# Kernel tuning notes

Hardware: AMD Instinct MI355X
Metric: run time of the kernel (lower is better)

Reference implementation:

```python
import jax, jax.numpy as jnp
import numpy as np

N_MET = 100_000
N_RXN = 50_000
E_SUB = 2_000_000
E_ALL = 4_000_000
MSG_DIM = 16
HIDDEN = 32


def setup_inputs() -> dict:
    key = jax.random.key(0)
    ks = jax.random.split(key, 16)
    x_met = jax.random.normal(ks[0], (N_MET,), dtype=jnp.float32)
    sto_sub = jax.random.uniform(ks[1], (E_SUB,), dtype=jnp.float32, minval=0.0, maxval=1.0)
    sto_all = jax.random.normal(ks[2], (E_ALL,), dtype=jnp.float32)
    met_sub = jax.random.randint(ks[3], (E_SUB,), 0, N_MET)
    rxn_sub = jax.random.randint(ks[4], (E_SUB,), 0, N_RXN)
    met_all = jax.random.randint(ks[5], (E_ALL,), 0, N_MET)
    rxn_all = jax.random.randint(ks[6], (E_ALL,), 0, N_RXN)
    # msg_mlp: Linear(2->HIDDEN), Tanh, Linear(HIDDEN->MSG_DIM)
    W1m = jax.random.normal(ks[7], (2, HIDDEN), jnp.float32) / np.sqrt(2.0)
    b1m = jnp.zeros((HIDDEN,), jnp.float32)
    W2m = jax.random.normal(ks[8], (HIDDEN, MSG_DIM), jnp.float32) / np.sqrt(HIDDEN)
    b2m = jnp.zeros((MSG_DIM,), jnp.float32)
    # rate_mlp: Linear(MSG_DIM->HIDDEN), Tanh, Linear(HIDDEN->1)
    W1r = jax.random.normal(ks[9], (MSG_DIM, HIDDEN), jnp.float32) / np.sqrt(MSG_DIM)
    b1r = jnp.zeros((HIDDEN,), jnp.float32)
    W2r = jax.random.normal(ks[10], (HIDDEN, 1), jnp.float32) / np.sqrt(HIDDEN)
    b2r = jnp.zeros((1,), jnp.float32)
    return {
        "x_met": x_met, "sto_sub": sto_sub, "sto_all": sto_all,
        "W1m": W1m, "b1m": b1m, "W2m": W2m, "b2m": b2m,
        "W1r": W1r, "b1r": b1r, "W2r": W2r, "b2r": b2r,
        "met_sub": met_sub, "rxn_sub": rxn_sub,
        "met_all": met_all, "rxn_all": rxn_all,
    }


def reference(x_met, sto_sub, sto_all, W1m, b1m, W2m, b2m, W1r, b1r, W2r, b2r,
              met_sub, rxn_sub, met_all, rxn_all):
    # gather substrate node features and build per-edge MLP input [E_sub, 2]
    msg_in = jnp.stack([x_met[met_sub], sto_sub], axis=-1)
    # msg MLP: tanh hidden, linear out -> [E_sub, MSG_DIM]
    msg = jnp.tanh(msg_in @ W1m + b1m) @ W2m + b2m
    # scatter-add messages into reactions -> [N_RXN, MSG_DIM]
    h_rxn = jax.ops.segment_sum(msg, rxn_sub, num_segments=N_RXN)
    # rate MLP + softplus -> per-reaction rate v [N_RXN]
    v = jax.nn.softplus((jnp.tanh(h_rxn @ W1r + b1r) @ W2r + b2r)[:, 0])
    # stoichiometric contributions scattered into metabolites -> dxdt [N_MET]
    contrib = sto_all * v[rxn_all]
    dxdt = jax.ops.segment_sum(contrib, met_all, num_segments=N_MET)
    return dxdt, v
```

## Files before the change

kernel.cpp:

```cpp
#include <hip/hip_runtime.h>

#define N_MET 100000
#define N_RXN 50000
#define E_SUB 2000000
#define E_ALL 4000000
#define MSG_DIM 16
#define HIDDEN 32

#define NBKT_A 391
#define NB_ALL 489
#define NBKT_S 782
#define NB_SUB 245


__device__ __forceinline__ float fast_tanh(float x) {
    const float ax = fabsf(x);
    const float e = __expf(2.0f * ax);
    const float t = 1.0f - 2.0f * __builtin_amdgcn_rcpf(e + 1.0f);
    return copysignf(t, x);
}


__global__ __launch_bounds__(1024) void hist_pair_kernel(
    const int* __restrict__ rxn_sub, const int* __restrict__ met_all,
    int* __restrict__ histS, int* __restrict__ histA)
{
    __shared__ int hb[NBKT_S];
    const int t = threadIdx.x, bk = blockIdx.x;
    if (bk < NB_SUB) {
        for (int i = t; i < NBKT_S; i += 1024) hb[i] = 0;
        __syncthreads();
#pragma unroll
        for (int k = 0; k < 2; ++k) {
            const int i = bk * 2048 + (k << 10) + t;
            if (i < E_SUB / 4) {
                const int4 r = ((const int4*)rxn_sub)[i];
                atomicAdd(&hb[r.x >> 6], 1);
                atomicAdd(&hb[r.y >> 6], 1);
                atomicAdd(&hb[r.z >> 6], 1);
                atomicAdd(&hb[r.w >> 6], 1);
            }
        }
        __syncthreads();
        for (int i = t; i < NBKT_S; i += 1024) histS[bk * NBKT_S + i] = hb[i];
    } else {
        const int ba = bk - NB_SUB;
        for (int i = t; i < NBKT_A; i += 1024) hb[i] = 0;
        __syncthreads();
#pragma unroll
        for (int k = 0; k < 2; ++k) {
            const int i = ba * 2048 + (k << 10) + t;
            if (i < E_ALL / 4) {
                const int4 m = ((const int4*)met_all)[i];
                atomicAdd(&hb[m.x >> 8], 1);
                atomicAdd(&hb[m.y >> 8], 1);
                atomicAdd(&hb[m.z >> 8], 1);
                atomicAdd(&hb[m.w >> 8], 1);
            }
        }
        __syncthreads();
        for (int i = t; i < NBKT_A; i += 1024) histA[ba * NBKT_A + i] = hb[i];
    }
}


__global__ __launch_bounds__(256) void scan_cols_pair_kernel(
    int* __restrict__ histS, int* __restrict__ histA,
    int* __restrict__ tot_s, int* __restrict__ tot_a)
{
    __shared__ int wsum[4];
    int* hist; int* tot; int nblocks, nbkt, b;
    if ((int)blockIdx.x < NBKT_S) {
        hist = histS; tot = tot_s; nblocks = NB_SUB; nbkt = NBKT_S;
        b = blockIdx.x;
    } else {
        hist = histA; tot = tot_a; nblocks = NB_ALL; nbkt = NBKT_A;
        b = blockIdx.x - NBKT_S;
    }
    const int t = threadIdx.x, lane = t & 63, w = t >> 6;
    int carry = 0;
    for (int basei = 0; basei < nblocks; basei += 256) {
        const int bk = basei + t;
        const int val = (bk < nblocks) ? hist[(size_t)bk * nbkt + b] : 0;
        int x = val;
#pragma unroll
        for (int off = 1; off < 64; off <<= 1) {
            const int y = __shfl_up(x, off);
            if (lane >= off) x += y;
        }
        if (lane == 63) wsum[w] = x;
        __syncthreads();
        if (w == 0) {
            int s = (lane < 4) ? wsum[lane] : 0;
#pragma unroll
            for (int off = 1; off < 4; off <<= 1) {
                const int y = __shfl_up(s, off);
                if (lane >= off) s += y;
            }
            if (lane < 4) wsum[lane] = s;
        }
        __syncthreads();
        const int excl = carry + ((w > 0) ? wsum[w - 1] : 0) + x - val;
        if (bk < nblocks) hist[(size_t)bk * nbkt + b] = excl;
        carry += wsum[3];
        __syncthreads();
    }
    if (t == 0) tot[b] = carry;
}

__global__ __launch_bounds__(256) void scan_base_pair_kernel(
    const int* __restrict__ tot_s, int* __restrict__ base_s,
    const int* __restrict__ tot_a, int* __restrict__ base_a)
{
    __shared__ int wsum[4];
    const int* tot; int* base; int nbkt;
    if (blockIdx.x == 0) { tot = tot_s; base = base_s; nbkt = NBKT_S; }
    else                 { tot = tot_a; base = base_a; nbkt = NBKT_A; }
    const int t = threadIdx.x, lane = t & 63, w = t >> 6;
    int carry = 0;
    for (int basei = 0; basei < nbkt; basei += 256) {
        const int i = basei + t;
        const int val = (i < nbkt) ? tot[i] : 0;
        int x = val;
#pragma unroll
        for (int off = 1; off < 64; off <<= 1) {
            const int y = __shfl_up(x, off);
            if (lane >= off) x += y;
        }
        if (lane == 63) wsum[w] = x;
        __syncthreads();
        if (w == 0) {
            int s = (lane < 4) ? wsum[lane] : 0;
#pragma unroll
            for (int off = 1; off < 4; off <<= 1) {
                const int y = __shfl_up(s, off);
                if (lane >= off) s += y;
            }
            if (lane < 4) wsum[lane] = s;
        }
        __syncthreads();
        const int excl = carry + ((w > 0) ? wsum[w - 1] : 0) + x - val;
        if (i < nbkt) base[i] = excl;
        carry += wsum[3];
        __syncthreads();
    }
}


__global__ __launch_bounds__(1024) void scatter_bin_sub_kernel(
    const float* __restrict__ x_met, const float* __restrict__ sto_sub,
    const int* __restrict__ met_sub, const int* __restrict__ rxn_sub,
    const int* __restrict__ hist, const int* __restrict__ base,
    float2* __restrict__ pxs)
{
    __shared__ float2 se[8192];
    __shared__ int cnt[NBKT_S];
    __shared__ int loff[NBKT_S + 1];
    __shared__ int goff[NBKT_S];
    const int t = threadIdx.x, bk = blockIdx.x;
    for (int i = t; i < NBKT_S; i += 1024) {
        cnt[i] = 0;
        goff[i] = hist[bk * NBKT_S + i] + base[i];
    }
    __syncthreads();

    float2 pay[8]; int meta[8];
    const int e0 = bk * 8192;
#pragma unroll
    for (int k = 0; k < 8; ++k) {
        const int e = e0 + (k << 10) + t;
        if (e < E_SUB) {
            const int r = rxn_sub[e];
            const float x = x_met[met_sub[e]];
            const int sb = (__float_as_int(sto_sub[e]) & ~63) | (r & 63);
            pay[k] = make_float2(x, __int_as_float(sb));
            const int q = r >> 6;
            meta[k] = (atomicAdd(&cnt[q], 1) << 10) | q;
        } else meta[k] = -1;
    }
    __syncthreads();

    if (t < 64) {
        int carry = 0;
        for (int bb = 0; bb < NBKT_S; bb += 64) {
            const int idx = bb + t;
            const int val = (idx < NBKT_S) ? cnt[idx] : 0;
            int x = val;
#pragma unroll
            for (int off = 1; off < 64; off <<= 1) {
                const int y = __shfl_up(x, off);
                if (t >= off) x += y;
            }
            if (idx < NBKT_S) loff[idx] = carry + x - val;
            carry += __shfl(x, 63);
        }
        if (t == 0) loff[NBKT_S] = carry;
    }
    __syncthreads();

#pragma unroll
    for (int k = 0; k < 8; ++k) {
        if (meta[k] >= 0)
            se[loff[meta[k] & 1023] + (meta[k] >> 10)] = pay[k];
    }
    __syncthreads();

    const int w = t >> 6, lane = t & 63;
    for (int q = w; q < NBKT_S; q += 16) {
        const int s = loff[q], lenq = loff[q + 1] - s, d = goff[q];
        for (int i = lane; i < lenq; i += 64)
            pxs[d + i] = se[s + i];
    }
}

__global__ __launch_bounds__(512, 6) void bucket_msg_kernel(
    const float2* __restrict__ pxs,
    const int* __restrict__ base, const int* __restrict__ tot,
    const float* __restrict__ W1m, const float* __restrict__ b1m,
    const float* __restrict__ W2m, const float* __restrict__ b2m,
    const float* __restrict__ W1r, const float* __restrict__ b1r,
    const float* __restrict__ W2r, const float* __restrict__ b2r,
    float* __restrict__ v)
{
    __shared__ float2 se[4096];
    __shared__ float  sth[64 * 33];
    __shared__ int    cnt[64];
    __shared__ int    soff[65];
    __shared__ int    ccnt[64];
    __shared__ float  sW2m[HIDDEN * MSG_DIM];
    __shared__ float  sb2m[MSG_DIM];
    __shared__ float  sW1r[MSG_DIM * HIDDEN];
    __shared__ float  sb1r[HIDDEN];
    __shared__ float  sW2r[HIDDEN];
    __shared__ float  sb2r;
    __shared__ float  sh[64 * 17];

    const int t = threadIdx.x;
    const int w = t >> 6, l = t & 63;
    const int half = l >> 5, j = l & 31;

    for (int i = t; i < HIDDEN * MSG_DIM; i += 512) sW2m[i] = W2m[i];
    for (int i = t; i < MSG_DIM * HIDDEN; i += 512) sW1r[i] = W1r[i];
    if (t < MSG_DIM) sb2m[t] = b2m[t];
    if (t < HIDDEN) sb1r[t] = b1r[t];
    if (t >= 64 && t < 64 + HIDDEN) sW2r[t - 64] = W2r[t - 64];
    if (t == 128) sb2r = b2r[0];
    if (t < 64) ccnt[t] = 0;

    const float w1x = W1m[j];
    const float w1y = W1m[HIDDEN + j];
    const float w1b = b1m[j];

    const int b = blockIdx.x;
    const int beg = base[b];
    const int end = beg + tot[b];

    float acc[4] = {0.0f, 0.0f, 0.0f, 0.0f};

    for (int cb = beg; cb < end; cb += 4096) {
        if (t < 64) cnt[t] = 0;
        __syncthreads();

        float2 pay[8];
        int meta[8];
#pragma unroll
        for (int k = 0; k < 8; ++k) {
            const int idx = cb + t + (k << 9);
            if (idx < end) {
                const float2 pv = pxs[idx];
                const int r = __float_as_int(pv.y) & 63;
                meta[k] = (atomicAdd(&cnt[r], 1) << 6) | r;
                pay[k] = pv;
            } else meta[k] = -1;
        }
        __syncthreads();

        if (t < 64) {
            const int orig = cnt[t];
            int x = orig;
#pragma unroll
            for (int off = 1; off < 64; off <<= 1) {
                const int y = __shfl_up(x, off);
                if (t >= off) x += y;
            }
            soff[t] = x - orig;
            if (t == 63) soff[64] = x;
            ccnt[t] += orig;
        }
        __syncthreads();

#pragma unroll
        for (int k = 0; k < 8; ++k) {
            if (meta[k] >= 0)
                se[soff[meta[k] & 63] + (meta[k] >> 6)] = pay[k];
        }
        __syncthreads();

#pragma unroll
        for (int p = 0; p < 4; ++p) {
            const int q = (w << 3) + (p << 1) + half;
            const int rb = soff[q];
            const int rl = soff[q + 1] - rb;
            float a0 = 0.0f, a1 = 0.0f;
            int i = 0;
            for (; i + 2 <= rl; i += 2) {
                const float2 e0 = se[rb + i];
                const float2 e1 = se[rb + i + 1];
                a0 += fast_tanh(fmaf(e0.x, w1x, fmaf(e0.y, w1y, w1b)));
                a1 += fast_tanh(fmaf(e1.x, w1x, fmaf(e1.y, w1y, w1b)));
            }
            if (i < rl) {
                const float2 e0 = se[rb + i];
                a0 += fast_tanh(fmaf(e0.x, w1x, fmaf(e0.y, w1y, w1b)));
            }
            acc[p] += a0 + a1;
        }
        __syncthreads();
    }

#pragma unroll
    for (int p = 0; p < 4; ++p) {
        const int q = (w << 3) + (p << 1) + half;
        sth[q * 33 + j] = acc[p];
    }
    __syncthreads();

    {
        const int r = t & 63, g = (t >> 6) << 1;
        const float cntf = (float)ccnt[r];
        float h0 = cntf * sb2m[g + 0], h1 = cntf * sb2m[g + 1];
#pragma unroll 8
        for (int jj = 0; jj < HIDDEN; ++jj) {
            const float ts = sth[r * 33 + jj];
            h0 = fmaf(ts, sW2m[jj * MSG_DIM + g + 0], h0);
            h1 = fmaf(ts, sW2m[jj * MSG_DIM + g + 1], h1);
        }
        sh[r * 17 + g + 0] = h0;
        sh[r * 17 + g + 1] = h1;
    }
    __syncthreads();

    if (t < 64) {
        const int r = b * 64 + t;
        if (r < N_RXN) {
            float h[MSG_DIM];
#pragma unroll
            for (int d = 0; d < MSG_DIM; ++d) h[d] = sh[t * 17 + d];
            float acc2 = sb2r;
#pragma unroll 2
            for (int jj = 0; jj < HIDDEN; ++jj) {
                float z = sb1r[jj];
#pragma unroll
                for (int d = 0; d < MSG_DIM; ++d)
                    z = fmaf(h[d], sW1r[d * HIDDEN + jj], z);
                acc2 = fmaf(fast_tanh(z), sW2r[jj], acc2);
            }
            v[r] = fmaxf(acc2, 0.0f) + log1pf(expf(-fabsf(acc2)));
        }
    }
}


__global__ __launch_bounds__(1024) void scatter_bin_kernel(
    const float* __restrict__ sto_all, const float* __restrict__ v,
    const int* __restrict__ met_all, const int* __restrict__ rxn_all,
    const int* __restrict__ hist, const int* __restrict__ base,
    float* __restrict__ pc)
{
    __shared__ float sp[8192];
    __shared__ int cnt[NBKT_A];
    __shared__ int loff[NBKT_A + 1];
    __shared__ int goff[NBKT_A];
    const int t = threadIdx.x, bk = blockIdx.x;
    for (int i = t; i < NBKT_A; i += 1024) {
        cnt[i] = 0;
        goff[i] = hist[bk * NBKT_A + i] + base[i];
    }
    __syncthreads();

    float pay[8]; int meta[8];
    const int e0 = bk * 8192;
#pragma unroll
    for (int k = 0; k < 8; ++k) {
        const int e = e0 + (k << 10) + t;
        if (e < E_ALL) {
            const int m = met_all[e];
            const float c = sto_all[e] * v[rxn_all[e]];
            const int cb = (__float_as_int(c) & ~255) | (m & 255);
            pay[k] = __int_as_float(cb);
            const int q = m >> 8;
            meta[k] = (atomicAdd(&cnt[q], 1) << 9) | q;
        } else meta[k] = -1;
    }
    __syncthreads();

    if (t < 64) {
        int carry = 0;
        for (int bb = 0; bb < NBKT_A; bb += 64) {
            const int idx = bb + t;
            const int val = (idx < NBKT_A) ? cnt[idx] : 0;
            int x = val;
#pragma unroll
            for (int off = 1; off < 64; off <<= 1) {
                const int y = __shfl_up(x, off);
                if (t >= off) x += y;
            }
            if (idx < NBKT_A) loff[idx] = carry + x - val;
            carry += __shfl(x, 63);
        }
        if (t == 0) loff[NBKT_A] = carry;
    }
    __syncthreads();

#pragma unroll
    for (int k = 0; k < 8; ++k) {
        if (meta[k] >= 0)
            sp[loff[meta[k] & 511] + (meta[k] >> 9)] = pay[k];
    }
    __syncthreads();

    const int w = t >> 6, lane = t & 63;
    for (int q = w; q < NBKT_A; q += 16) {
        const int s = loff[q], lenq = loff[q + 1] - s, d = goff[q];
        for (int i = lane; i < lenq; i += 64)
            pc[d + i] = sp[s + i];
    }
}

__global__ __launch_bounds__(512) void bucket_accum_kernel(
    const float* __restrict__ pc,
    const int* __restrict__ base, const int* __restrict__ tot,
    float* __restrict__ dxdt)
{
    __shared__ float acc[256];
    const int b = blockIdx.x, t = threadIdx.x;
    if (t < 256) acc[t] = 0.0f;
    __syncthreads();
    const int beg = base[b];
    const int end = beg + tot[b];
    for (int i = beg + t; i < end; i += 512) {
        const float pv = pc[i];
        atomicAdd(&acc[__float_as_int(pv) & 255], pv);
    }
    __syncthreads();
    if (t < 256) {
        const int met = b * 256 + t;
        if (met < N_MET) dxdt[met] = acc[t];
    }
}

extern "C" void kernel_launch(void* const* d_in, const int* in_sizes, int n_in,
                              void* d_out, int out_size, void* d_ws, size_t ws_size,
                              hipStream_t stream) {
    const float* x_met   = (const float*)d_in[0];
    const float* sto_sub = (const float*)d_in[1];
    const float* sto_all = (const float*)d_in[2];
    const float* W1m     = (const float*)d_in[3];
    const float* b1m     = (const float*)d_in[4];
    const float* W2m     = (const float*)d_in[5];
    const float* b2m     = (const float*)d_in[6];
    const float* W1r     = (const float*)d_in[7];
    const float* b1r     = (const float*)d_in[8];
    const float* W2r     = (const float*)d_in[9];
    const float* b2r     = (const float*)d_in[10];
    const int*   met_sub = (const int*)d_in[11];
    const int*   rxn_sub = (const int*)d_in[12];
    const int*   met_all = (const int*)d_in[13];
    const int*   rxn_all = (const int*)d_in[14];

    float* dxdt = (float*)d_out;
    float* v    = dxdt + N_MET;

    char* ws = (char*)d_ws;
    int* histS  = (int*)ws;  ws += (((size_t)NB_SUB * NBKT_S * 4 + 15) / 16) * 16;
    int* histA  = (int*)ws;  ws += (((size_t)NB_ALL * NBKT_A * 4 + 15) / 16) * 16;
    int* tot_s  = (int*)ws;  ws += ((sizeof(int) * NBKT_S + 15) / 16) * 16;
    int* base_s = (int*)ws;  ws += ((sizeof(int) * NBKT_S + 15) / 16) * 16;
    int* tot_a  = (int*)ws;  ws += ((sizeof(int) * NBKT_A + 15) / 16) * 16;
    int* base_a = (int*)ws;  ws += ((sizeof(int) * NBKT_A + 15) / 16) * 16;
    char* P = ws;
    float2* pxs = (float2*)P;
    float*  pc  = (float*)P;

    hist_pair_kernel<<<NB_SUB + NB_ALL, 1024, 0, stream>>>(
        rxn_sub, met_all, histS, histA);
    scan_cols_pair_kernel<<<NBKT_S + NBKT_A, 256, 0, stream>>>(
        histS, histA, tot_s, tot_a);
    scan_base_pair_kernel<<<2, 256, 0, stream>>>(tot_s, base_s, tot_a, base_a);

    scatter_bin_sub_kernel<<<NB_SUB, 1024, 0, stream>>>(
        x_met, sto_sub, met_sub, rxn_sub, histS, base_s, pxs);
    bucket_msg_kernel<<<NBKT_S, 512, 0, stream>>>(
        pxs, base_s, tot_s, W1m, b1m, W2m, b2m, W1r, b1r, W2r, b2r, v);

    scatter_bin_kernel<<<NB_ALL, 1024, 0, stream>>>(
        sto_all, v, met_all, rxn_all, histA, base_a, pc);
    bucket_accum_kernel<<<NBKT_A, 512, 0, stream>>>(pc, base_a, tot_a, dxdt);
}
```

Baseline: 272.0 us.

## Merge scan kernels with last-block pattern, enlarge all-edge tiles, vectorize loads

Folds the base scan into the column-scan kernel using an atomic counter, so the last finishing block computes bucket bases and one launch disappears. Doubles the tile size of the all-edge scatter to 16384 so both scatter paths use 245 blocks. That kernel now does the histogram pass on met_all first and reads rxn_all/sto_all in a second pass with int4/float4 loads, and the substrate scatter and bucket accumulation also switch to 128-bit loads. The costs are fewer, heavier blocks with more shared memory each, a device-scope threadfence, and a reordered edge-to-thread mapping.

```diff
diff --git a/kernel.cpp b/kernel.cpp
--- a/kernel.cpp
+++ b/kernel.cpp
@@ -8,9 +8,12 @@
 #define HIDDEN 32
 
 #define NBKT_A 391
-#define NB_ALL 489
+#define NB_ALL 245
+#define TILE_A 16384
 #define NBKT_S 782
 #define NB_SUB 245
+#define TILE_S 8192
+#define NSCAN (NBKT_S + NBKT_A)
 
 
 __device__ __forceinline__ float fast_tanh(float x) {
@@ -23,10 +26,11 @@
 
 __global__ __launch_bounds__(1024) void hist_pair_kernel(
     const int* __restrict__ rxn_sub, const int* __restrict__ met_all,
-    int* __restrict__ histS, int* __restrict__ histA)
+    int* __restrict__ histS, int* __restrict__ histA, int* __restrict__ ctr)
 {
     __shared__ int hb[NBKT_S];
     const int t = threadIdx.x, bk = blockIdx.x;
+    if (bk == 0 && t == 0) *ctr = 0;
     if (bk < NB_SUB) {
         for (int i = t; i < NBKT_S; i += 1024) hb[i] = 0;
         __syncthreads();
@@ -48,8 +52,8 @@
         for (int i = t; i < NBKT_A; i += 1024) hb[i] = 0;
         __syncthreads();
 #pragma unroll
-        for (int k = 0; k < 2; ++k) {
-            const int i = ba * 2048 + (k << 10) + t;
+        for (int k = 0; k < 4; ++k) {
+            const int i = ba * 4096 + (k << 10) + t;
             if (i < E_ALL / 4) {
                 const int4 m = ((const int4*)met_all)[i];
                 atomicAdd(&hb[m.x >> 8], 1);
@@ -64,24 +68,15 @@
 }
 
 
-__global__ __launch_bounds__(256) void scan_cols_pair_kernel(
-    int* __restrict__ histS, int* __restrict__ histA,
-    int* __restrict__ tot_s, int* __restrict__ tot_a)
-{
-    __shared__ int wsum[4];
-    int* hist; int* tot; int nblocks, nbkt, b;
-    if ((int)blockIdx.x < NBKT_S) {
-        hist = histS; tot = tot_s; nblocks = NB_SUB; nbkt = NBKT_S;
-        b = blockIdx.x;
-    } else {
-        hist = histA; tot = tot_a; nblocks = NB_ALL; nbkt = NBKT_A;
-        b = blockIdx.x - NBKT_S;
-    }
-    const int t = threadIdx.x, lane = t & 63, w = t >> 6;
+__device__ __forceinline__ void excl_scan_small(
+    const int* __restrict__ tot, int* __restrict__ base, int n,
+    int t, int* wsum)
+{
+    const int lane = t & 63, w = t >> 6;
     int carry = 0;
-    for (int basei = 0; basei < nblocks; basei += 256) {
-        const int bk = basei + t;
-        const int val = (bk < nblocks) ? hist[(size_t)bk * nbkt + b] : 0;
+    for (int basei = 0; basei < n; basei += 256) {
+        const int i = basei + t;
+        const int val = (i < n) ? tot[i] : 0;
         int x = val;
 #pragma unroll
         for (int off = 1; off < 64; off <<= 1) {
@@ -100,50 +95,57 @@
             if (lane < 4) wsum[lane] = s;
         }
         __syncthreads();
-        const int excl = carry + ((w > 0) ? wsum[w - 1] : 0) + x - val;
-        if (bk < nblocks) hist[(size_t)bk * nbkt + b] = excl;
+        if (i < n) base[i] = carry + ((w > 0) ? wsum[w - 1] : 0) + x - val;
         carry += wsum[3];
         __syncthreads();
     }
-    if (t == 0) tot[b] = carry;
-}
-
-__global__ __launch_bounds__(256) void scan_base_pair_kernel(
-    const int* __restrict__ tot_s, int* __restrict__ base_s,
-    const int* __restrict__ tot_a, int* __restrict__ base_a)
+}
+
+__global__ __launch_bounds__(256) void scan_cols_pair_kernel(
+    int* __restrict__ histS, int* __restrict__ histA,
+    int* __restrict__ tot_s, int* __restrict__ tot_a,
+    int* __restrict__ base_s, int* __restrict__ base_a,
+    int* __restrict__ ctr)
 {
     __shared__ int wsum[4];
-    const int* tot; int* base; int nbkt;
-    if (blockIdx.x == 0) { tot = tot_s; base = base_s; nbkt = NBKT_S; }
-    else                 { tot = tot_a; base = base_a; nbkt = NBKT_A; }
+    __shared__ int is_last;
+    int* hist; int* tot; int nbkt, b;
+    if ((int)blockIdx.x < NBKT_S) {
+        hist = histS; tot = tot_s; nbkt = NBKT_S; b = blockIdx.x;
+    } else {
+        hist = histA; tot = tot_a; nbkt = NBKT_A; b = blockIdx.x - NBKT_S;
+    }
     const int t = threadIdx.x, lane = t & 63, w = t >> 6;
-    int carry = 0;
-    for (int basei = 0; basei < nbkt; basei += 256) {
-        const int i = basei + t;
-        const int val = (i < nbkt) ? tot[i] : 0;
-        int x = val;
-#pragma unroll
-        for (int off = 1; off < 64; off <<= 1) {
-            const int y = __shfl_up(x, off);
-            if (lane >= off) x += y;
-        }
-        if (lane == 63) wsum[w] = x;
-        __syncthreads();
-        if (w == 0) {
-            int s = (lane < 4) ? wsum[lane] : 0;
-#pragma unroll
-            for (int off = 1; off < 4; off <<= 1) {
-                const int y = __shfl_up(s, off);
-                if (lane >= off) s += y;
-            }
-            if (lane < 4) wsum[lane] = s;
-        }
-        __syncthreads();
-        const int excl = carry + ((w > 0) ? wsum[w - 1] : 0) + x - val;
-        if (i < nbkt) base[i] = excl;
-        carry += wsum[3];
-        __syncthreads();
-    }
+    const int val = (t < 245) ? hist[(size_t)t * nbkt + b] : 0;
+    int x = val;
+#pragma unroll
+    for (int off = 1; off < 64; off <<= 1) {
+        const int y = __shfl_up(x, off);
+        if (lane >= off) x += y;
+    }
+    if (lane == 63) wsum[w] = x;
+    __syncthreads();
+    if (w == 0) {
+        int s = (lane < 4) ? wsum[lane] : 0;
+#pragma unroll
+        for (int off = 1; off < 4; off <<= 1) {
+            const int y = __shfl_up(s, off);
+            if (lane >= off) s += y;
+        }
+        if (lane < 4) wsum[lane] = s;
+    }
+    __syncthreads();
+    const int excl = ((w > 0) ? wsum[w - 1] : 0) + x - val;
+    if (t < 245) hist[(size_t)t * nbkt + b] = excl;
+    if (t == 0) tot[b] = wsum[3];
+
+    __threadfence();
+    if (t == 0) is_last = (atomicAdd(ctr, 1) == NSCAN - 1) ? 1 : 0;
+    __syncthreads();
+    if (!is_last) return;
+    __threadfence();
+    excl_scan_small(tot_s, base_s, NBKT_S, t, wsum);
+    excl_scan_small(tot_a, base_a, NBKT_A, t, wsum);
 }
 
 
@@ -153,7 +155,7 @@
     const int* __restrict__ hist, const int* __restrict__ base,
     float2* __restrict__ pxs)
 {
-    __shared__ float2 se[8192];
+    __shared__ float2 se[TILE_S];
     __shared__ int cnt[NBKT_S];
     __shared__ int loff[NBKT_S + 1];
     __shared__ int goff[NBKT_S];
@@ -164,19 +166,42 @@
     }
     __syncthreads();
 
+    const int e0 = bk * TILE_S;
+    const int rem = min(TILE_S, E_SUB - e0);
+    const int tb = 8 * t;
     float2 pay[8]; int meta[8];
-    const int e0 = bk * 8192;
-#pragma unroll
-    for (int k = 0; k < 8; ++k) {
-        const int e = e0 + (k << 10) + t;
-        if (e < E_SUB) {
-            const int r = rxn_sub[e];
-            const float x = x_met[met_sub[e]];
-            const int sb = (__float_as_int(sto_sub[e]) & ~63) | (r & 63);
+    if (tb + 8 <= rem) {
+        const int4 r01 = ((const int4*)(rxn_sub + e0))[2 * t];
+        const int4 r23 = ((const int4*)(rxn_sub + e0))[2 * t + 1];
+        const int4 m01 = ((const int4*)(met_sub + e0))[2 * t];
+        const int4 m23 = ((const int4*)(met_sub + e0))[2 * t + 1];
+        const float4 s01 = ((const float4*)(sto_sub + e0))[2 * t];
+        const float4 s23 = ((const float4*)(sto_sub + e0))[2 * t + 1];
+        const int rr[8] = {r01.x, r01.y, r01.z, r01.w, r23.x, r23.y, r23.z, r23.w};
+        const int mm[8] = {m01.x, m01.y, m01.z, m01.w, m23.x, m23.y, m23.z, m23.w};
+        const float ss[8] = {s01.x, s01.y, s01.z, s01.w, s23.x, s23.y, s23.z, s23.w};
+#pragma unroll
+        for (int k = 0; k < 8; ++k) {
+            const int r = rr[k];
+            const float x = x_met[mm[k]];
+            const int sb = (__float_as_int(ss[k]) & ~63) | (r & 63);
             pay[k] = make_float2(x, __int_as_float(sb));
             const int q = r >> 6;
             meta[k] = (atomicAdd(&cnt[q], 1) << 10) | q;
-        } else meta[k] = -1;
+        }
+    } else {
+#pragma unroll
+        for (int k = 0; k < 8; ++k) {
+            const int e = e0 + tb + k;
+            if (e < E_SUB) {
+                const int r = rxn_sub[e];
+                const float x = x_met[met_sub[e]];
+                const int sb = (__float_as_int(sto_sub[e]) & ~63) | (r & 63);
+                pay[k] = make_float2(x, __int_as_float(sb));
+                const int q = r >> 6;
+                meta[k] = (atomicAdd(&cnt[q], 1) << 10) | q;
+            } else meta[k] = -1;
+        }
     }
     __syncthreads();
 
@@ -367,7 +392,7 @@
     const int* __restrict__ hist, const int* __restrict__ base,
     float* __restrict__ pc)
 {
-    __shared__ float sp[8192];
+    __shared__ float sp[TILE_A];
     __shared__ int cnt[NBKT_A];
     __shared__ int loff[NBKT_A + 1];
     __shared__ int goff[NBKT_A];
@@ -378,19 +403,29 @@
     }
     __syncthreads();
 
-    float pay[8]; int meta[8];
-    const int e0 = bk * 8192;
-#pragma unroll
-    for (int k = 0; k < 8; ++k) {
-        const int e = e0 + (k << 10) + t;
-        if (e < E_ALL) {
-            const int m = met_all[e];
-            const float c = sto_all[e] * v[rxn_all[e]];
-            const int cb = (__float_as_int(c) & ~255) | (m & 255);
-            pay[k] = __int_as_float(cb);
-            const int q = m >> 8;
-            meta[k] = (atomicAdd(&cnt[q], 1) << 9) | q;
-        } else meta[k] = -1;
+    const int e0 = bk * TILE_A;
+    const int rem = min(TILE_A, E_ALL - e0);
+    const int tb = 16 * t;
+    int meta[16];
+    const bool full = (tb + 16 <= rem);
+    if (full) {
+#pragma unroll
+        for (int kk = 0; kk < 4; ++kk) {
+            const int4 m = ((const int4*)(met_all + e0))[4 * t + kk];
+            meta[4 * kk + 0] = (atomicAdd(&cnt[m.x >> 8], 1) << 17) | m.x;
+            meta[4 * kk + 1] = (atomicAdd(&cnt[m.y >> 8], 1) << 17) | m.y;
+            meta[4 * kk + 2] = (atomicAdd(&cnt[m.z >> 8], 1) << 17) | m.z;
+            meta[4 * kk + 3] = (atomicAdd(&cnt[m.w >> 8], 1) << 17) | m.w;
+        }
+    } else {
+#pragma unroll
+        for (int k = 0; k < 16; ++k) {
+            const int e = e0 + tb + k;
+            if (e < E_ALL) {
+                const int m = met_all[e];
+                meta[k] = (atomicAdd(&cnt[m >> 8], 1) << 17) | m;
+            } else meta[k] = -1;
+        }
     }
     __syncthreads();
 
@@ -412,10 +447,34 @@
     }
     __syncthreads();
 
-#pragma unroll
-    for (int k = 0; k < 8; ++k) {
-        if (meta[k] >= 0)
-            sp[loff[meta[k] & 511] + (meta[k] >> 9)] = pay[k];
+    if (full) {
+#pragma unroll
+        for (int kk = 0; kk < 4; ++kk) {
+            const int4 r = ((const int4*)(rxn_all + e0))[4 * t + kk];
+            const float4 s = ((const float4*)(sto_all + e0))[4 * t + kk];
+            const int rr[4] = {r.x, r.y, r.z, r.w};
+            const float ss[4] = {s.x, s.y, s.z, s.w};
+#pragma unroll
+            for (int u = 0; u < 4; ++u) {
+                const int mt = meta[4 * kk + u];
+                const int m = mt & 0x1FFFF;
+                const float c = ss[u] * v[rr[u]];
+                const int cb = (__float_as_int(c) & ~255) | (m & 255);
+                sp[loff[m >> 8] + (mt >> 17)] = __int_as_float(cb);
+            }
+        }
+    } else {
+#pragma unroll
+        for (int k = 0; k < 16; ++k) {
+            const int e = e0 + tb + k;
+            if (e < E_ALL) {
+                const int mt = meta[k];
+                const int m = mt & 0x1FFFF;
+                const float c = sto_all[e] * v[rxn_all[e]];
+                const int cb = (__float_as_int(c) & ~255) | (m & 255);
+                sp[loff[m >> 8] + (mt >> 17)] = __int_as_float(cb);
+            }
+        }
     }
     __syncthreads();
 
@@ -438,7 +497,21 @@
     __syncthreads();
     const int beg = base[b];
     const int end = beg + tot[b];
-    for (int i = beg + t; i < end; i += 512) {
+    int a0 = (beg + 3) & ~3;
+    if (a0 > end) a0 = end;
+    const int a1 = a0 + ((end - a0) & ~3);
+    for (int i = beg + t; i < a0; i += 512) {
+        const float pv = pc[i];
+        atomicAdd(&acc[__float_as_int(pv) & 255], pv);
+    }
+    for (int i = a0 + 4 * t; i < a1; i += 2048) {
+        const float4 pv = *(const float4*)(pc + i);
+        atomicAdd(&acc[__float_as_int(pv.x) & 255], pv.x);
+        atomicAdd(&acc[__float_as_int(pv.y) & 255], pv.y);
+        atomicAdd(&acc[__float_as_int(pv.z) & 255], pv.z);
+        atomicAdd(&acc[__float_as_int(pv.w) & 255], pv.w);
+    }
+    for (int i = a1 + t; i < end; i += 512) {
         const float pv = pc[i];
         atomicAdd(&acc[__float_as_int(pv) & 255], pv);
     }
@@ -478,15 +551,15 @@
     int* base_s = (int*)ws;  ws += ((sizeof(int) * NBKT_S + 15) / 16) * 16;
     int* tot_a  = (int*)ws;  ws += ((sizeof(int) * NBKT_A + 15) / 16) * 16;
     int* base_a = (int*)ws;  ws += ((sizeof(int) * NBKT_A + 15) / 16) * 16;
+    int* ctr    = (int*)ws;  ws += 16;
     char* P = ws;
     float2* pxs = (float2*)P;
     float*  pc  = (float*)P;
 
     hist_pair_kernel<<<NB_SUB + NB_ALL, 1024, 0, stream>>>(
-        rxn_sub, met_all, histS, histA);
-    scan_cols_pair_kernel<<<NBKT_S + NBKT_A, 256, 0, stream>>>(
-        histS, histA, tot_s, tot_a);
-    scan_base_pair_kernel<<<2, 256, 0, stream>>>(tot_s, base_s, tot_a, base_a);
+        rxn_sub, met_all, histS, histA, ctr);
+    scan_cols_pair_kernel<<<NSCAN, 256, 0, stream>>>(
+        histS, histA, tot_s, tot_a, base_s, base_a, ctr);
 
     scatter_bin_sub_kernel<<<NB_SUB, 1024, 0, stream>>>(
         x_met, sto_sub, met_sub, rxn_sub, histS, base_s, pxs);
```

Result: slower. 419.8 us (+54.3%).
